# Kernel optimization log

Measured on AMD Instinct MI355X. Metric: run time of the kernel, lower is better.

## Reference

```python
import jax, jax.numpy as jnp
import numpy as np
import math

EMBED_DIM = 1024
NUM_HEADS = 16
DEPTH = 12
HEAD_DIM = EMBED_DIM // NUM_HEADS // 2  # 32
LAMBDA_INIT = 0.8 - 0.6 * math.exp(-0.3 * DEPTH)
SCALE = HEAD_DIM ** -0.5  # flash_attn default softmax scale
RMS_EPS = 1e-5
BATCH, SEQ = 2, 2048


def _freqs(seq_len):
    # angle = 1 / 10000 ** linspace(0, 1, head_dim//2); freqs = pos * angle
    angle = 1.0 / 10000.0 ** jnp.linspace(0.0, 1.0, HEAD_DIM // 2)
    idx = jnp.arange(seq_len, dtype=jnp.float32)
    f = idx[:, None] * angle[None, :]
    return jnp.cos(f), jnp.sin(f)


def _rope_interleaved(x, cos, sin):
    # x: (b, t, h, d); cos/sin: (t, d//2). Interleaved pairs (0,1),(2,3),...
    x1, x2 = x[..., 0::2], x[..., 1::2]
    c = cos[None, :, None, :]
    s = sin[None, :, None, :]
    o1 = x1 * c - x2 * s
    o2 = x1 * s + x2 * c
    return jnp.stack([o1, o2], axis=-1).reshape(x.shape)


def _forward(x, Wq, Wk, Wv, Wo, lambda_q1, lambda_k1, lambda_q2, lambda_k2, rms_weight):
    b, t, _ = x.shape
    q = (x @ Wq.T).reshape(b, t, 2 * NUM_HEADS, HEAD_DIM)
    k = (x @ Wk.T).reshape(b, t, 2 * NUM_HEADS, HEAD_DIM)
    v = (x @ Wv.T).reshape(b, t, NUM_HEADS, 2, HEAD_DIM)
    cos, sin = _freqs(t)
    q = _rope_interleaved(q, cos, sin)
    k = _rope_interleaved(k, cos, sin)
    # split the 2H axis into (H, 2): q1/q2 are even/odd sub-heads
    q = q.reshape(b, t, NUM_HEADS, 2, HEAD_DIM)
    k = k.reshape(b, t, NUM_HEADS, 2, HEAD_DIM)
    q1, q2 = q[..., 0, :], q[..., 1, :]
    k1, k2 = k[..., 0, :], k[..., 1, :]
    v12 = v.reshape(b, t, NUM_HEADS, 2 * HEAD_DIM)  # == concat(v1, v2) on last dim

    def attend(qh, kh):
        scores = jnp.einsum('bthd,bshd->bhts', qh, kh) * SCALE
        p = jax.nn.softmax(scores, axis=-1)  # non-causal, as in source
        return jnp.einsum('bhts,bshe->bthe', p, v12)  # (b, t, H, 2*hd)

    attn1 = attend(q1, k1)
    attn2 = attend(q2, k2)
    lam = (jnp.exp(jnp.sum(lambda_q1 * lambda_k1))
           - jnp.exp(jnp.sum(lambda_q2 * lambda_k2)) + LAMBDA_INIT)
    a = attn1 - lam * attn2
    # RMSNorm over last dim (2*head_dim) with affine weight
    a = a * jax.lax.rsqrt(jnp.mean(a * a, axis=-1, keepdims=True) + RMS_EPS) * rms_weight
    a = a * (1.0 - LAMBDA_INIT)
    a = a.reshape(b, t, NUM_HEADS * 2 * HEAD_DIM)
    return a @ Wo.T


def setup_inputs() -> dict:
    key = jax.random.key(0)
    ks = jax.random.split(key, 9)
    std = EMBED_DIM ** -0.5
    return {
        'x': jax.random.normal(ks[0], (BATCH, SEQ, EMBED_DIM), jnp.float32),
        'Wq': jax.random.normal(ks[1], (EMBED_DIM, EMBED_DIM), jnp.float32) * std,
        'Wk': jax.random.normal(ks[2], (EMBED_DIM, EMBED_DIM), jnp.float32) * std,
        'Wv': jax.random.normal(ks[3], (EMBED_DIM, EMBED_DIM), jnp.float32) * std,
        'Wo': jax.random.normal(ks[4], (EMBED_DIM, EMBED_DIM), jnp.float32) * std,
        'lambda_q1': jax.random.normal(ks[5], (HEAD_DIM,), jnp.float32) * 0.1,
        'lambda_k1': jax.random.normal(ks[6], (HEAD_DIM,), jnp.float32) * 0.1,
        'lambda_q2': jax.random.normal(ks[7], (HEAD_DIM,), jnp.float32) * 0.1,
        'lambda_k2': jax.random.normal(ks[8], (HEAD_DIM,), jnp.float32) * 0.1,
        'rms_weight': jnp.ones((2 * HEAD_DIM,), jnp.float32),
    }


def reference(x, Wq, Wk, Wv, Wo, lambda_q1, lambda_k1, lambda_q2, lambda_k2, rms_weight):
    return _forward(x, Wq, Wk, Wv, Wo, lambda_q1, lambda_k1, lambda_q2, lambda_k2, rms_weight)
```

## Files before the change

### kernel.cpp

```cpp
#include <hip/hip_runtime.h>
#include <stdint.h>

typedef unsigned short u16;
typedef __bf16 bf16x8 __attribute__((ext_vector_type(8)));
typedef float f32x4 __attribute__((ext_vector_type(4)));

#define TOKENS 4096
#define SEQLEN 2048
#define EMB 1024
#define NHEADS 16

static constexpr float LAMBDA_INIT_F = 0.7836057665316245f;
static constexpr float ONE_MINUS_LI  = 0.21639423346837553f;
static constexpr float SCALE_F       = 0.17677669529663687f;
static constexpr float LOG2E_F       = 1.4426950408889634f;

__device__ __forceinline__ u16 f2bf(float f) {
  uint32_t u = __builtin_bit_cast(uint32_t, f);
  u += 0x7fffu + ((u >> 16) & 1u);
  return (u16)(u >> 16);
}
__device__ __forceinline__ float bf2f(u16 h) {
  uint32_t u = ((uint32_t)h) << 16;
  return __builtin_bit_cast(float, u);
}
__device__ __forceinline__ float fast_exp2(float x) {
#if __has_builtin(__builtin_amdgcn_exp2f)
  return __builtin_amdgcn_exp2f(x);
#else
  return exp2f(x);
#endif
}
__device__ __forceinline__ void async16(const void* g, void* l) {
  __builtin_amdgcn_global_load_lds((__attribute__((address_space(1))) void*)(g),
                                   (__attribute__((address_space(3))) void*)(l),
                                   16, 0, 0);
}
__device__ __forceinline__ f32x4 mfma16(uint4 a, uint4 b, f32x4 c) {
  return __builtin_amdgcn_mfma_f32_16x16x32_bf16(
      __builtin_bit_cast(bf16x8, a), __builtin_bit_cast(bf16x8, b), c, 0, 0, 0);
}

__global__ __launch_bounds__(256) void prep_kernel(
    const float* __restrict__ x,  const float* __restrict__ wq,
    const float* __restrict__ wk, const float* __restrict__ wv,
    const float* __restrict__ wo, const float* __restrict__ lq1,
    const float* __restrict__ lk1,const float* __restrict__ lq2,
    const float* __restrict__ lk2,
    u16* __restrict__ xb, u16* __restrict__ wqb, u16* __restrict__ wkb,
    u16* __restrict__ wvb, u16* __restrict__ wob, float* __restrict__ lam_out)
{
  int i0 = (blockIdx.x * 256 + threadIdx.x) * 4;
  const float* src; u16* dst; int j;
  if (i0 < 4194304)      { src = x;  dst = xb;  j = i0; }
  else if (i0 < 5242880) { src = wq; dst = wqb; j = i0 - 4194304; }
  else if (i0 < 6291456) { src = wk; dst = wkb; j = i0 - 5242880; }
  else if (i0 < 7340032) { src = wv; dst = wvb; j = i0 - 6291456; }
  else                   { src = wo; dst = wob; j = i0 - 7340032; }
  float4 v = *(const float4*)(src + j);
  uint2 pack;
  pack.x = (uint32_t)f2bf(v.x) | ((uint32_t)f2bf(v.y) << 16);
  pack.y = (uint32_t)f2bf(v.z) | ((uint32_t)f2bf(v.w) << 16);
  *(uint2*)(dst + j) = pack;

  if (blockIdx.x == 0 && threadIdx.x == 0) {
    float d1 = 0.f, d2 = 0.f;
    for (int i = 0; i < 32; ++i) { d1 += lq1[i] * lk1[i]; d2 += lq2[i] * lk2[i]; }
    *lam_out = expf(d1) - expf(d2) + LAMBDA_INIT_F;
  }
}

template <int MODE>
__device__ __forceinline__ void gemm_body(const u16* __restrict__ A,
                                          const u16* __restrict__ B,
                                          void* __restrict__ C)
{
  __shared__ u16 As[128 * 64];
  __shared__ u16 Bs[128 * 64];
  const int t = threadIdx.x;
  const int lane = t & 63, w = t >> 6;
  const int q4 = lane >> 4, lm = lane & 15;
  const int wr = w >> 1, wc = w & 1;
  const int bm = blockIdx.y * 128, bn = blockIdx.x * 128;

  f32x4 acc[4][4];
#pragma unroll
  for (int mi = 0; mi < 4; ++mi)
#pragma unroll
    for (int ni = 0; ni < 4; ++ni) acc[mi][ni] = (f32x4){0.f, 0.f, 0.f, 0.f};

  for (int kt = 0; kt < 16; ++kt) {
    const int k0 = kt * 64;
    __syncthreads();
#pragma unroll
    for (int ro = 0; ro < 4; ++ro) {
      int ft = ro * 256 + t;
      int row = ft >> 3;
      int col = (((ft & 7) ^ (row & 7)) << 3);
      async16(&A[(bm + row) * 1024 + k0 + col], &As[ft * 8]);
      async16(&B[(bn + row) * 1024 + k0 + col], &Bs[ft * 8]);
    }
    __syncthreads();
#pragma unroll
    for (int ks = 0; ks < 2; ++ks) {
      uint4 af[4], bf[4];
#pragma unroll
      for (int mi = 0; mi < 4; ++mi)
        af[mi] = *(const uint4*)&As[(wr * 64 + mi * 16 + lm) * 64 +
                                    (((ks * 4 + q4) ^ (lm & 7)) << 3)];
#pragma unroll
      for (int ni = 0; ni < 4; ++ni)
        bf[ni] = *(const uint4*)&Bs[(wc * 64 + ni * 16 + lm) * 64 +
                                    (((ks * 4 + q4) ^ (lm & 7)) << 3)];
#pragma unroll
      for (int mi = 0; mi < 4; ++mi)
#pragma unroll
        for (int ni = 0; ni < 4; ++ni)
          acc[mi][ni] = mfma16(af[mi], bf[ni], acc[mi][ni]);
    }
  }
#pragma unroll
  for (int mi = 0; mi < 4; ++mi)
#pragma unroll
    for (int ni = 0; ni < 4; ++ni) {
      if (MODE == 2) {
        int token0 = bm + wr * 64 + mi * 16 + q4 * 4;
        int col = bn + wc * 64 + ni * 16 + lm;
        int bb = token0 >> 11, key0 = token0 & 2047;
        int h = col >> 6, d = col & 63;
        ushort4 pk;
        pk.x = f2bf(acc[mi][ni][0]);
        pk.y = f2bf(acc[mi][ni][1]);
        pk.z = f2bf(acc[mi][ni][2]);
        pk.w = f2bf(acc[mi][ni][3]);
        *(ushort4*)((u16*)C + ((size_t)((bb * 16 + h) * 64 + d)) * 2048 + key0) = pk;
      } else {
#pragma unroll
        for (int r = 0; r < 4; ++r) {
          int row = bm + wr * 64 + mi * 16 + q4 * 4 + r;
          int col = bn + wc * 64 + ni * 16 + lm;
          if (MODE == 1) ((float*)C)[row * 1024 + col] = acc[mi][ni][r];
          else           ((u16*)C)[row * 1024 + col]   = f2bf(acc[mi][ni][r]);
        }
      }
    }
}

__global__ __launch_bounds__(256) void gemm_qkv_kernel(
    const u16* __restrict__ xb, const u16* __restrict__ wqb,
    const u16* __restrict__ wkb, const u16* __restrict__ wvb,
    u16* __restrict__ qb, u16* __restrict__ kb, u16* __restrict__ vtb)
{
  if (blockIdx.z == 0)      gemm_body<0>(xb, wqb, qb);
  else if (blockIdx.z == 1) gemm_body<0>(xb, wkb, kb);
  else                      gemm_body<2>(xb, wvb, vtb);
}

__global__ __launch_bounds__(256) void gemm_out_kernel(
    const u16* __restrict__ ab, const u16* __restrict__ wob,
    float* __restrict__ out)
{
  gemm_body<1>(ab, wob, out);
}

__global__ __launch_bounds__(256) void rope_kernel(u16* __restrict__ qb,
                                                   u16* __restrict__ kb)
{
  int p = blockIdx.x * 256 + threadIdx.x;
  int tok = p >> 9;
  int pc = p & 511;
  int j = pc & 15;
  int tpos = tok & (SEQLEN - 1);
  float ang = exp2f(-(float)j * 0.8858474919699633f);
  float f = (float)tpos * ang;
  float s, c;
  sincosf(f, &s, &c);
  u16* ptr = ((blockIdx.y == 0) ? qb : kb) + tok * 1024 + pc * 2;
  uint32_t u = *(const uint32_t*)ptr;
  float x1 = bf2f((u16)(u & 0xffff));
  float x2 = bf2f((u16)(u >> 16));
  float o1 = x1 * c - x2 * s;
  float o2 = x1 * s + x2 * c;
  if (blockIdx.y == 0) { o1 *= SCALE_F * LOG2E_F; o2 *= SCALE_F * LOG2E_F; }
  *(uint32_t*)ptr = (uint32_t)f2bf(o1) | ((uint32_t)f2bf(o2) << 16);
}

__global__ __launch_bounds__(256) void attn_kernel(
    const u16* __restrict__ qb, const u16* __restrict__ kb,
    const u16* __restrict__ vtb, const float* __restrict__ lam_p,
    const float* __restrict__ rmsw, u16* __restrict__ ab)
{
  __shared__ u16 smem[17408];

  const int t = threadIdx.x;
  const int lane = t & 63, w = t >> 6;
  const int q4 = lane >> 4, lm = lane & 15;
  const int qt = blockIdx.x, h = blockIdx.y, b = blockIdx.z;
  const int tok0 = b * SEQLEN + qt * 64;
  const int hch = h * 64;

  const u16* kbase = kb + (size_t)(b * SEQLEN) * 1024 + hch;
  const u16* vbase = vtb + (size_t)((b * 16 + h) * 64) * 2048;

#pragma unroll
  for (int ro = 0; ro < 2; ++ro) {
    int ft = ro * 256 + t;
    int row = ft >> 3;
    int col = (((ft & 7) ^ (row & 7)) << 3);
    async16(&qb[(tok0 + row) * 1024 + hch + col], &smem[8192 + ft * 8]);
  }
  __syncthreads();
  uint4 qf[2];
#pragma unroll
  for (int c = 0; c < 2; ++c)
    qf[c] = *(const uint4*)&smem[8192 + (w * 16 + lm) * 64 +
                                 (((c * 4 + q4) ^ (lm & 7)) << 3)];

  const f32x4 fzero = {0.f, 0.f, 0.f, 0.f};
  const uint4 ones = {0x3F803F80u, 0x3F803F80u, 0x3F803F80u, 0x3F803F80u};
  f32x4 O[2][4];
  f32x4 ls[2];
#pragma unroll
  for (int c = 0; c < 2; ++c) {
    ls[c] = fzero;
#pragma unroll
    for (int ni = 0; ni < 4; ++ni) O[c][ni] = fzero;
  }

  for (int kv = 0; kv < SEQLEN; kv += 64) {
    __syncthreads();
#pragma unroll
    for (int ro = 0; ro < 2; ++ro) {
      int ft = ro * 256 + t;
      int row = ft >> 3;
      int col = (((ft & 7) ^ (row & 7)) << 3);
      async16(kbase + (kv + row) * 1024 + col, &smem[ft * 8]);
      async16(vbase + row * 2048 + kv + col, &smem[4096 + ft * 8]);
    }
    __syncthreads();

#pragma unroll
    for (int c = 0; c < 2; ++c) {
      f32x4 s4[4];
#pragma unroll
      for (int ni = 0; ni < 4; ++ni) {
        uint4 kf = *(const uint4*)&smem[(ni * 16 + lm) * 64 +
                                        (((c * 4 + q4) ^ (lm & 7)) << 3)];
        s4[ni] = mfma16(qf[c], kf, fzero);
      }
      u16* P = &smem[8192 + c * 4608];
#pragma unroll
      for (int ni = 0; ni < 4; ++ni)
#pragma unroll
        for (int r = 0; r < 4; ++r)
          P[(w * 16 + q4 * 4 + r) * 72 + ni * 16 + lm] = f2bf(fast_exp2(s4[ni][r]));
    }

#pragma unroll
    for (int kb2 = 0; kb2 < 2; ++kb2) {
      uint4 vf[4];
#pragma unroll
      for (int ni = 0; ni < 4; ++ni)
        vf[ni] = *(const uint4*)&smem[4096 + (ni * 16 + lm) * 64 +
                                      (((kb2 * 4 + q4) ^ (lm & 7)) << 3)];
#pragma unroll
      for (int c = 0; c < 2; ++c) {
        uint4 af = *(const uint4*)&smem[8192 + c * 4608 + (w * 16 + lm) * 72 +
                                        (kb2 * 4 + q4) * 8];
        ls[c] = mfma16(af, ones, ls[c]);
#pragma unroll
        for (int ni = 0; ni < 4; ++ni)
          O[c][ni] = mfma16(af, vf[ni], O[c][ni]);
      }
    }
  }

  float lam = *lam_p;
  float inv1[4], inv2[4];
#pragma unroll
  for (int r = 0; r < 4; ++r) {
    inv1[r] = 1.f / ls[0][r];
    inv2[r] = lam / ls[1][r];
  }
  f32x4 a4[4];
#pragma unroll
  for (int ni = 0; ni < 4; ++ni)
#pragma unroll
    for (int r = 0; r < 4; ++r)
      a4[ni][r] = O[0][ni][r] * inv1[r] - O[1][ni][r] * inv2[r];
  float ssq[4] = {0.f, 0.f, 0.f, 0.f};
#pragma unroll
  for (int ni = 0; ni < 4; ++ni)
#pragma unroll
    for (int r = 0; r < 4; ++r) ssq[r] += a4[ni][r] * a4[ni][r];
#pragma unroll
  for (int off = 8; off > 0; off >>= 1) {
#pragma unroll
    for (int r = 0; r < 4; ++r) ssq[r] += __shfl_xor(ssq[r], off);
  }
  float sc[4];
#pragma unroll
  for (int r = 0; r < 4; ++r)
    sc[r] = rsqrtf(ssq[r] * (1.f / 64.f) + 1e-5f) * ONE_MINUS_LI;
  float wv4[4];
#pragma unroll
  for (int ni = 0; ni < 4; ++ni) wv4[ni] = rmsw[ni * 16 + lm];
#pragma unroll
  for (int ni = 0; ni < 4; ++ni)
#pragma unroll
    for (int r = 0; r < 4; ++r) {
      int row = tok0 + w * 16 + q4 * 4 + r;
      int col = hch + ni * 16 + lm;
      ab[row * 1024 + col] = f2bf(a4[ni][r] * sc[r] * wv4[ni]);
    }
}

extern "C" void kernel_launch(void* const* d_in, const int* in_sizes, int n_in,
                              void* d_out, int out_size, void* d_ws, size_t ws_size,
                              hipStream_t stream)
{
  (void)in_sizes; (void)n_in; (void)out_size; (void)ws_size;
  const float* x    = (const float*)d_in[0];
  const float* Wq   = (const float*)d_in[1];
  const float* Wk   = (const float*)d_in[2];
  const float* Wv   = (const float*)d_in[3];
  const float* Wo   = (const float*)d_in[4];
  const float* lq1  = (const float*)d_in[5];
  const float* lk1  = (const float*)d_in[6];
  const float* lq2  = (const float*)d_in[7];
  const float* lk2  = (const float*)d_in[8];
  const float* rmsw = (const float*)d_in[9];
  float* out = (float*)d_out;

  char* ws = (char*)d_ws;
  u16* xb   = (u16*)(ws + 0);
  u16* wqb  = (u16*)(ws + 8388608);
  u16* wkb  = (u16*)(ws + 10485760);
  u16* wvb  = (u16*)(ws + 12582912);
  u16* wob  = (u16*)(ws + 14680064);
  u16* qb   = (u16*)(ws + 16777216);
  u16* kb   = (u16*)(ws + 25165824);
  u16* vtb  = (u16*)(ws + 33554432);
  u16* ab   = (u16*)(ws + 41943040);
  float* lam = (float*)(ws + 50331648);

  hipLaunchKernelGGL(prep_kernel, dim3(8192), dim3(256), 0, stream,
                     x, Wq, Wk, Wv, Wo, lq1, lk1, lq2, lk2,
                     xb, wqb, wkb, wvb, wob, lam);
  hipLaunchKernelGGL(gemm_qkv_kernel, dim3(8, 32, 3), dim3(256), 0, stream,
                     xb, wqb, wkb, wvb, qb, kb, vtb);
  hipLaunchKernelGGL(rope_kernel, dim3(8192, 2), dim3(256), 0, stream, qb, kb);
  hipLaunchKernelGGL(attn_kernel, dim3(32, 16, 2), dim3(256), 0, stream,
                     qb, kb, vtb, lam, rmsw, ab);
  hipLaunchKernelGGL(gemm_out_kernel, dim3(8, 32, 1), dim3(256), 0, stream,
                     ab, wob, out);
}
```

Baseline: 279.2 us.

## Switch attention to 32x32 MFMA tiles with 128-query blocks

Rewrites the attention kernel to use 32x32x16 bf16 MFMA instead of 16x16x32. Each block now handles 128 queries (32 per wave), which halves the grid and doubles K/V reuse per LDS load. Scores are computed transposed (K as A operand), so P is written to a per-wave swizzled LDS buffer with packed bf16 truncation via perm. Row sums are accumulated in registers instead of by an extra MFMA against a ones vector. Risks include higher register pressure from 32x32 accumulators, truncating rather than rounding P to bf16, and fewer blocks (512) to fill the CUs.

```diff
diff --git a/kernel.cpp b/kernel.cpp
--- a/kernel.cpp
+++ b/kernel.cpp
@@ -4,6 +4,7 @@
 typedef unsigned short u16;
 typedef __bf16 bf16x8 __attribute__((ext_vector_type(8)));
 typedef float f32x4 __attribute__((ext_vector_type(4)));
+typedef float f32x16 __attribute__((ext_vector_type(16)));
 
 #define TOKENS 4096
 #define SEQLEN 2048
@@ -38,6 +39,10 @@
 }
 __device__ __forceinline__ f32x4 mfma16(uint4 a, uint4 b, f32x4 c) {
   return __builtin_amdgcn_mfma_f32_16x16x32_bf16(
+      __builtin_bit_cast(bf16x8, a), __builtin_bit_cast(bf16x8, b), c, 0, 0, 0);
+}
+__device__ __forceinline__ f32x16 mfma32(uint4 a, uint4 b, f32x16 c) {
+  return __builtin_amdgcn_mfma_f32_32x32x16_bf16(
       __builtin_bit_cast(bf16x8, a), __builtin_bit_cast(bf16x8, b), c, 0, 0, 0);
 }
 
@@ -190,42 +195,44 @@
     const u16* __restrict__ vtb, const float* __restrict__ lam_p,
     const float* __restrict__ rmsw, u16* __restrict__ ab)
 {
-  __shared__ u16 smem[17408];
+  __shared__ u16 smem[16384];
 
   const int t = threadIdx.x;
   const int lane = t & 63, w = t >> 6;
-  const int q4 = lane >> 4, lm = lane & 15;
+  const int l5 = lane >> 5, lr = lane & 31;
   const int qt = blockIdx.x, h = blockIdx.y, b = blockIdx.z;
-  const int tok0 = b * SEQLEN + qt * 64;
+  const int tok0 = b * SEQLEN + qt * 128;
   const int hch = h * 64;
 
   const u16* kbase = kb + (size_t)(b * SEQLEN) * 1024 + hch;
   const u16* vbase = vtb + (size_t)((b * 16 + h) * 64) * 2048;
-
-#pragma unroll
-  for (int ro = 0; ro < 2; ++ro) {
+  u16* P = &smem[8192 + w * 2048];
+
+#pragma unroll
+  for (int ro = 0; ro < 4; ++ro) {
     int ft = ro * 256 + t;
     int row = ft >> 3;
     int col = (((ft & 7) ^ (row & 7)) << 3);
     async16(&qb[(tok0 + row) * 1024 + hch + col], &smem[8192 + ft * 8]);
   }
   __syncthreads();
-  uint4 qf[2];
+  uint4 qf[2][2];
 #pragma unroll
   for (int c = 0; c < 2; ++c)
-    qf[c] = *(const uint4*)&smem[8192 + (w * 16 + lm) * 64 +
-                                 (((c * 4 + q4) ^ (lm & 7)) << 3)];
-
-  const f32x4 fzero = {0.f, 0.f, 0.f, 0.f};
-  const uint4 ones = {0x3F803F80u, 0x3F803F80u, 0x3F803F80u, 0x3F803F80u};
-  f32x4 O[2][4];
-  f32x4 ls[2];
-#pragma unroll
-  for (int c = 0; c < 2; ++c) {
-    ls[c] = fzero;
-#pragma unroll
-    for (int ni = 0; ni < 4; ++ni) O[c][ni] = fzero;
-  }
+#pragma unroll
+    for (int kk = 0; kk < 2; ++kk)
+      qf[c][kk] = *(const uint4*)&smem[8192 + (w * 32 + lr) * 64 +
+                                       (((c * 4 + kk * 2 + l5) ^ (lr & 7)) << 3)];
+
+  f32x16 O[2][2];
+#pragma unroll
+  for (int c = 0; c < 2; ++c)
+#pragma unroll
+    for (int n = 0; n < 2; ++n)
+#pragma unroll
+      for (int i = 0; i < 16; ++i) O[c][n][i] = 0.f;
+  float rs[2] = {0.f, 0.f};
+  uint4 vf[2][4];
 
   for (int kv = 0; kv < SEQLEN; kv += 64) {
     __syncthreads();
@@ -241,78 +248,76 @@
 
 #pragma unroll
     for (int c = 0; c < 2; ++c) {
-      f32x4 s4[4];
-#pragma unroll
-      for (int ni = 0; ni < 4; ++ni) {
-        uint4 kf = *(const uint4*)&smem[(ni * 16 + lm) * 64 +
-                                        (((c * 4 + q4) ^ (lm & 7)) << 3)];
-        s4[ni] = mfma16(qf[c], kf, fzero);
+#pragma unroll
+      for (int kb2 = 0; kb2 < 2; ++kb2) {
+        f32x16 s;
+#pragma unroll
+        for (int i = 0; i < 16; ++i) s[i] = 0.f;
+#pragma unroll
+        for (int kk = 0; kk < 2; ++kk) {
+          uint4 kf = *(const uint4*)&smem[(kb2 * 32 + lr) * 64 +
+                                          (((c * 4 + kk * 2 + l5) ^ (lr & 7)) << 3)];
+          s = mfma32(kf, qf[c][kk], s);
+        }
+        float rloc = 0.f;
+#pragma unroll
+        for (int g = 0; g < 4; ++g) {
+          float e0 = fast_exp2(s[g * 4 + 0]);
+          float e1 = fast_exp2(s[g * 4 + 1]);
+          float e2 = fast_exp2(s[g * 4 + 2]);
+          float e3 = fast_exp2(s[g * 4 + 3]);
+          rloc += (e0 + e1) + (e2 + e3);
+          uint2 pk;
+          pk.x = __builtin_amdgcn_perm(__builtin_bit_cast(uint32_t, e1),
+                                       __builtin_bit_cast(uint32_t, e0), 0x07060302u);
+          pk.y = __builtin_amdgcn_perm(__builtin_bit_cast(uint32_t, e3),
+                                       __builtin_bit_cast(uint32_t, e2), 0x07060302u);
+          *(uint2*)&P[lr * 64 + ((((kb2 * 4 + g) ^ (lr & 7)) << 3) + l5 * 4)] = pk;
+        }
+        rs[c] += rloc;
       }
-      u16* P = &smem[8192 + c * 4608];
-#pragma unroll
-      for (int ni = 0; ni < 4; ++ni)
-#pragma unroll
-        for (int r = 0; r < 4; ++r)
-          P[(w * 16 + q4 * 4 + r) * 72 + ni * 16 + lm] = f2bf(fast_exp2(s4[ni][r]));
-    }
-
-#pragma unroll
-    for (int kb2 = 0; kb2 < 2; ++kb2) {
-      uint4 vf[4];
-#pragma unroll
-      for (int ni = 0; ni < 4; ++ni)
-        vf[ni] = *(const uint4*)&smem[4096 + (ni * 16 + lm) * 64 +
-                                      (((kb2 * 4 + q4) ^ (lm & 7)) << 3)];
-#pragma unroll
-      for (int c = 0; c < 2; ++c) {
-        uint4 af = *(const uint4*)&smem[8192 + c * 4608 + (w * 16 + lm) * 72 +
-                                        (kb2 * 4 + q4) * 8];
-        ls[c] = mfma16(af, ones, ls[c]);
-#pragma unroll
-        for (int ni = 0; ni < 4; ++ni)
-          O[c][ni] = mfma16(af, vf[ni], O[c][ni]);
+      if (c == 0) {
+#pragma unroll
+        for (int n = 0; n < 2; ++n)
+#pragma unroll
+          for (int kc = 0; kc < 4; ++kc)
+            vf[n][kc] = *(const uint4*)&smem[4096 + (n * 32 + lr) * 64 +
+                                             (((kc * 2 + l5) ^ (lr & 7)) << 3)];
       }
+#pragma unroll
+      for (int kc = 0; kc < 4; ++kc) {
+        uint4 af = *(const uint4*)&P[lr * 64 + (((kc * 2 + l5) ^ (lr & 7)) << 3)];
+        O[c][0] = mfma32(af, vf[0][kc], O[c][0]);
+        O[c][1] = mfma32(af, vf[1][kc], O[c][1]);
+      }
     }
   }
 
   float lam = *lam_p;
-  float inv1[4], inv2[4];
-#pragma unroll
-  for (int r = 0; r < 4; ++r) {
-    inv1[r] = 1.f / ls[0][r];
-    inv2[r] = lam / ls[1][r];
-  }
-  f32x4 a4[4];
-#pragma unroll
-  for (int ni = 0; ni < 4; ++ni)
-#pragma unroll
-    for (int r = 0; r < 4; ++r)
-      a4[ni][r] = O[0][ni][r] * inv1[r] - O[1][ni][r] * inv2[r];
-  float ssq[4] = {0.f, 0.f, 0.f, 0.f};
-#pragma unroll
-  for (int ni = 0; ni < 4; ++ni)
-#pragma unroll
-    for (int r = 0; r < 4; ++r) ssq[r] += a4[ni][r] * a4[ni][r];
-#pragma unroll
-  for (int off = 8; off > 0; off >>= 1) {
-#pragma unroll
-    for (int r = 0; r < 4; ++r) ssq[r] += __shfl_xor(ssq[r], off);
-  }
-  float sc[4];
-#pragma unroll
-  for (int r = 0; r < 4; ++r)
-    sc[r] = rsqrtf(ssq[r] * (1.f / 64.f) + 1e-5f) * ONE_MINUS_LI;
-  float wv4[4];
-#pragma unroll
-  for (int ni = 0; ni < 4; ++ni) wv4[ni] = rmsw[ni * 16 + lm];
-#pragma unroll
-  for (int ni = 0; ni < 4; ++ni)
-#pragma unroll
-    for (int r = 0; r < 4; ++r) {
-      int row = tok0 + w * 16 + q4 * 4 + r;
-      int col = hch + ni * 16 + lm;
-      ab[row * 1024 + col] = f2bf(a4[ni][r] * sc[r] * wv4[ni]);
-    }
+  rs[0] += __shfl_xor(rs[0], 32);
+  rs[1] += __shfl_xor(rs[1], 32);
+  float inv1 = 1.f / rs[0];
+  float inv2 = lam / rs[1];
+  float wv2[2] = { rmsw[lr], rmsw[32 + lr] };
+#pragma unroll
+  for (int g = 0; g < 4; ++g) {
+#pragma unroll
+    for (int rr = 0; rr < 4; ++rr) {
+      int r = g * 4 + rr;
+      int qrl = rr + 8 * g + 4 * l5;
+      float i1 = __shfl(inv1, qrl);
+      float i2 = __shfl(inv2, qrl);
+      float a0 = O[0][0][r] * i1 - O[1][0][r] * i2;
+      float a1 = O[0][1][r] * i1 - O[1][1][r] * i2;
+      float ssq = a0 * a0 + a1 * a1;
+#pragma unroll
+      for (int off = 16; off > 0; off >>= 1) ssq += __shfl_xor(ssq, off);
+      float sc = rsqrtf(ssq * (1.f / 64.f) + 1e-5f) * ONE_MINUS_LI;
+      int row = tok0 + w * 32 + qrl;
+      ab[row * 1024 + hch + lr]      = f2bf(a0 * sc * wv2[0]);
+      ab[row * 1024 + hch + 32 + lr] = f2bf(a1 * sc * wv2[1]);
+    }
+  }
 }
 
 extern "C" void kernel_launch(void* const* d_in, const int* in_sizes, int n_in,
@@ -350,7 +355,7 @@
   hipLaunchKernelGGL(gemm_qkv_kernel, dim3(8, 32, 3), dim3(256), 0, stream,
                      xb, wqb, wkb, wvb, qb, kb, vtb);
   hipLaunchKernelGGL(rope_kernel, dim3(8192, 2), dim3(256), 0, stream, qb, kb);
-  hipLaunchKernelGGL(attn_kernel, dim3(32, 16, 2), dim3(256), 0, stream,
+  hipLaunchKernelGGL(attn_kernel, dim3(16, 16, 2), dim3(256), 0, stream,
                      qb, kb, vtb, lam, rmsw, ab);
   hipLaunchKernelGGL(gemm_out_kernel, dim3(8, 32, 1), dim3(256), 0, stream,
                      ab, wob, out);
```

Measured after the change: 252.8 us. -9.5%, faster.
